# Performance work log

Measured on AMD Instinct MI355X. Metric: run time of the kernel, lower is better.

## Reference

```python
import jax, jax.numpy as jnp
import numpy as np
from jax import lax

DN = ('NHWC', 'HWIO', 'NHWC')
OUTPUT_STRIDE = 2
PEAK_THRESHOLD = 0.2


def setup_inputs() -> dict:
    key = jax.random.key(0)
    k1, k2, k3 = jax.random.split(key, 3)
    crops = jax.random.normal(k1, (128, 192, 192, 1), dtype=jnp.float32)
    # simple confmap backbone: stride-2 conv -> relu -> 3x3 conv to 17 nodes
    W1 = jax.random.normal(k2, (3, 3, 1, 32), dtype=jnp.float32) * 0.1
    b1 = jnp.zeros((32,), dtype=jnp.float32)
    W2 = jax.random.normal(k3, (3, 3, 32, 17), dtype=jnp.float32) * 0.1
    b2 = jnp.zeros((17,), dtype=jnp.float32)
    return {"crops": crops, "W1": W1, "b1": b1, "W2": W2, "b2": b2}


def _confmaps(crops, W1, b1, W2, b2):
    # keras_model forward: (B, 192, 192, 1) -> (B, 96, 96, 17), output_stride = 2
    h = lax.conv_general_dilated(crops, W1, (2, 2), 'SAME', dimension_numbers=DN) + b1
    h = jax.nn.relu(h)
    cms = lax.conv_general_dilated(h, W2, (1, 1), 'SAME', dimension_numbers=DN) + b2
    return cms


def _find_global_peaks_local(cms, threshold):
    # cms: (B, H, W, N) -> peaks (B, N, 2) in (x, y), vals (B, N)
    B, H, W, N = cms.shape
    cm = jnp.transpose(cms, (0, 3, 1, 2)).reshape(B, N, H * W)  # (B, N, HW)
    flat_idx = jnp.argmax(cm, axis=-1)                           # (B, N)
    vals = jnp.take_along_axis(cm, flat_idx[..., None], axis=-1)[..., 0]
    yi = flat_idx // W
    xi = flat_idx % W

    def gather(yy, xx):
        yy = jnp.clip(yy, 0, H - 1)
        xx = jnp.clip(xx, 0, W - 1)
        return jnp.take_along_axis(cm, (yy * W + xx)[..., None], axis=-1)[..., 0]

    # quarter-pixel local gradient offset (refinement='local')
    dx = 0.25 * jnp.sign(gather(yi, xi + 1) - gather(yi, xi - 1))
    dy = 0.25 * jnp.sign(gather(yi + 1, xi) - gather(yi - 1, xi))

    pts = jnp.stack([xi.astype(cm.dtype) + dx, yi.astype(cm.dtype) + dy], axis=-1)
    pts = jnp.where(vals[..., None] >= threshold, pts, jnp.nan)
    return pts, vals


def reference(crops, W1, b1, W2, b2):
    # preprocess: inputs already float grayscale, input_scale=1.0 -> identity
    cms = _confmaps(crops, W1, b1, W2, b2)
    peak_points, peak_vals = _find_global_peaks_local(cms, PEAK_THRESHOLD)
    peak_points = peak_points * OUTPUT_STRIDE  # adjust to input image grid
    # pack (x, y, val) into one array: (B, nodes, 3)
    return jnp.concatenate([peak_points, peak_vals[..., None]], axis=-1)
```

## Files before the change

### kernel.cpp

```cpp
#include <hip/hip_runtime.h>


#define NCH 17
#define C1 32
#define TS2 32
#define HT2 34
#define HS 36
#define IN2 69
#define CG 4
#define NG 8

__device__ __forceinline__ unsigned long long pack_key(float v, unsigned flat) {
    unsigned ub = __float_as_uint(v);
    ub = (ub & 0x80000000u) ? ~ub : (ub | 0x80000000u);
    return ((unsigned long long)ub << 32) | (unsigned)(~flat);
}

__global__ __launch_bounds__(256, 4) void conv_peaks_kernel(
    const float* __restrict__ crops, const float* __restrict__ W1g,
    const float* __restrict__ b1g, const float* __restrict__ W2g,
    const float* __restrict__ b2g, unsigned long long* __restrict__ peaks) {
    __shared__ float s_in[IN2 * IN2];
    __shared__ __align__(16) float s_h[CG * HT2 * HS];

    const int t = threadIdx.x;
    const int b = blockIdx.y;
    const int ty0 = (blockIdx.x / 3) * TS2;
    const int tx0 = (blockIdx.x % 3) * TS2;
    const int iy0 = 2 * ty0 - 2;
    const int ix0 = 2 * tx0 - 2;
    const float* cb = crops + b * 192 * 192;

    for (int p = t; p < IN2 * IN2; p += 256) {
        int r = p / IN2, cc = p - r * IN2;
        int iy = iy0 + r, ix = ix0 + cc;
        float v = 0.f;
        if (iy >= 0 && ix >= 0 && iy < 192 && ix < 192) v = cb[iy * 192 + ix];
        s_in[p] = v;
    }

    const int ly = t >> 3;
    const int lx0 = (t & 7) * 4;
    float acc[NCH][4];
#pragma unroll
    for (int n = 0; n < NCH; ++n)
#pragma unroll
        for (int p = 0; p < 4; ++p) acc[n][p] = 0.f;

#pragma unroll 1
    for (int g = 0; g < NG; ++g) {
        __syncthreads();

        for (int p = t; p < HT2 * HT2; p += 256) {
            int r = p / HT2, cc = p - r * HT2;
            int hy = ty0 - 1 + r, hx = tx0 - 1 + cc;
            bool valid = (hy >= 0) && (hy < 96) && (hx >= 0) && (hx < 96);
            float in9[9];
#pragma unroll
            for (int q = 0; q < 9; ++q)
                in9[q] = s_in[(2 * r + q / 3) * IN2 + (2 * cc + q % 3)];
#pragma unroll
            for (int cl = 0; cl < CG; ++cl) {
                int c = g * CG + cl;
                float a = b1g[c];
#pragma unroll
                for (int q = 0; q < 9; ++q) a = fmaf(in9[q], W1g[q * C1 + c], a);
                a = valid ? fmaxf(a, 0.f) : 0.f;
                s_h[cl * (HT2 * HS) + r * HS + cc] = a;
            }
        }
        __syncthreads();

#pragma unroll 1
        for (int cl = 0; cl < CG; ++cl) {
            float hrow[3][6];
            const float* hp = s_h + cl * (HT2 * HS) + ly * HS + lx0;
#pragma unroll
            for (int r = 0; r < 3; ++r) {
                float4 h4 = *(const float4*)(hp + r * HS);
                float2 h2 = *(const float2*)(hp + r * HS + 4);
                hrow[r][0] = h4.x; hrow[r][1] = h4.y;
                hrow[r][2] = h4.z; hrow[r][3] = h4.w;
                hrow[r][4] = h2.x; hrow[r][5] = h2.y;
            }
            const int c = g * CG + cl;
#pragma unroll
            for (int k = 0; k < 9; ++k) {
                const int ky = k / 3, kx = k - ky * 3;
                const float* wb = W2g + (k * C1 + c) * NCH;
                float w[NCH];
#pragma unroll
                for (int n = 0; n < NCH; ++n) w[n] = wb[n];
#pragma unroll
                for (int n = 0; n < NCH; ++n)
#pragma unroll
                    for (int p = 0; p < 4; ++p)
                        acc[n][p] = fmaf(hrow[ky][kx + p], w[n], acc[n][p]);
            }
        }
    }

    const int yg = ty0 + ly, xg = tx0 + lx0;
    const int lane = t & 63;
#pragma unroll
    for (int n = 0; n < NCH; ++n) {
        float bb = b2g[n];
        unsigned long long pk = pack_key(acc[n][0] + bb, (unsigned)(yg * 96 + xg));
#pragma unroll
        for (int p = 1; p < 4; ++p) {
            unsigned long long o = pack_key(acc[n][p] + bb, (unsigned)(yg * 96 + xg + p));
            if (o > pk) pk = o;
        }
#pragma unroll
        for (int off = 32; off; off >>= 1) {
            unsigned long long o = __shfl_down(pk, off, 64);
            if (o > pk) pk = o;
        }
        if (lane == 0) atomicMax(&peaks[b * NCH + n], pk);
    }
}

__global__ __launch_bounds__(64) void refine_kernel(
    const float* __restrict__ crops, const float* __restrict__ W1g,
    const float* __restrict__ b1g, const float* __restrict__ W2g,
    const unsigned long long* __restrict__ peaks, float* __restrict__ out) {
    const int bn = blockIdx.x;
    const int b = bn / NCH, n = bn % NCH;
    const int lane = threadIdx.x;

    unsigned long long pk = peaks[bn];
    unsigned key = (unsigned)(pk >> 32);
    unsigned fbits = (key & 0x80000000u) ? (key ^ 0x80000000u) : ~key;
    float val = __uint_as_float(fbits);
    int flat = (int)(~(unsigned)(pk & 0xffffffffu));
    int yi = flat / 96, xi = flat - yi * 96;

    const int j = lane >> 4;
    int yy = yi + ((j == 2) ? 1 : 0) - ((j == 3) ? 1 : 0);
    int xx = xi + ((j == 0) ? 1 : 0) - ((j == 1) ? 1 : 0);
    yy = min(max(yy, 0), 95);
    xx = min(max(xx, 0), 95);

    const float* cb = crops + b * 192 * 192;
    float pat[7][7];
#pragma unroll
    for (int r = 0; r < 7; ++r) {
        int iy = 2 * yy - 2 + r;
#pragma unroll
        for (int s = 0; s < 7; ++s) {
            int ix = 2 * xx - 2 + s;
            pat[r][s] = (iy >= 0 && iy < 192 && ix >= 0 && ix < 192)
                            ? cb[iy * 192 + ix] : 0.f;
        }
    }

    float part = 0.f;
#pragma unroll
    for (int ci = 0; ci < 2; ++ci) {
        const int c = (lane & 15) + ci * 16;
        const float bias = b1g[c];
        float w1[9];
#pragma unroll
        for (int q = 0; q < 9; ++q) w1[q] = W1g[q * C1 + c];
#pragma unroll
        for (int dy = 0; dy < 3; ++dy) {
#pragma unroll
            for (int dx = 0; dx < 3; ++dx) {
                int hy = yy - 1 + dy, hx = xx - 1 + dx;
                if (hy >= 0 && hy < 96 && hx >= 0 && hx < 96) {
                    float a = bias;
#pragma unroll
                    for (int qy = 0; qy < 3; ++qy)
#pragma unroll
                        for (int qx = 0; qx < 3; ++qx)
                            a = fmaf(pat[2 * dy + qy][2 * dx + qx],
                                     w1[qy * 3 + qx], a);
                    float hval = fmaxf(a, 0.f);
                    part = fmaf(hval, W2g[((dy * 3 + dx) * C1 + c) * NCH + n], part);
                }
            }
        }
    }
    for (int off = 8; off; off >>= 1) part += __shfl_down(part, off, 16);
    float g0 = __shfl(part, 0, 64);
    float g1 = __shfl(part, 16, 64);
    float g2 = __shfl(part, 32, 64);
    float g3 = __shfl(part, 48, 64);

    if (lane == 0) {
        float d0 = g0 - g1, d1 = g2 - g3;
        float sx = (d0 > 0.f) ? 1.f : ((d0 < 0.f) ? -1.f : 0.f);
        float sy = (d1 > 0.f) ? 1.f : ((d1 < 0.f) ? -1.f : 0.f);
        float px = ((float)xi + 0.25f * sx) * 2.f;
        float py = ((float)yi + 0.25f * sy) * 2.f;
        if (!(val >= 0.2f)) {
            px = __int_as_float(0x7fc00000);
            py = __int_as_float(0x7fc00000);
        }
        out[bn * 3 + 0] = px;
        out[bn * 3 + 1] = py;
        out[bn * 3 + 2] = val;
    }
}

extern "C" void kernel_launch(void* const* d_in, const int* in_sizes, int n_in,
                              void* d_out, int out_size, void* d_ws, size_t ws_size,
                              hipStream_t stream) {
    const float* crops = (const float*)d_in[0];
    const float* W1 = (const float*)d_in[1];
    const float* b1 = (const float*)d_in[2];
    const float* W2 = (const float*)d_in[3];
    const float* b2 = (const float*)d_in[4];
    float* out = (float*)d_out;
    unsigned long long* peaks = (unsigned long long*)d_ws;

    hipMemsetAsync(d_ws, 0, 128 * NCH * sizeof(unsigned long long), stream);

    dim3 gridB(9, 128);
    conv_peaks_kernel<<<gridB, 256, 0, stream>>>(crops, W1, b1, W2, b2, peaks);
    refine_kernel<<<128 * NCH, 64, 0, stream>>>(crops, W1, b1, W2, peaks, out);
}
```

Baseline: 222.3 us.

## Use packed FP32 FMAs and smaller 24x32 tiles for more blocks

Conv2 accumulation now runs on two-wide float vectors (v_pk_fma_f32 on CDNA) over 16 of the 17 output channels, with a scalar FMA for the last one. This targets the FMA issue bottleneck of the second convolution. The tile shrinks to 24x32 with 3 pixels per thread, which raises the grid from 9 to 12 blocks per image to fill more CUs. The trade-off is more halo recompute of conv1 per output pixel and scalar rather than vectorized LDS loads.

```diff
diff --git a/kernel.cpp b/kernel.cpp
--- a/kernel.cpp
+++ b/kernel.cpp
@@ -3,12 +3,17 @@
 
 #define NCH 17
 #define C1 32
-#define TS2 32
-#define HT2 34
-#define HS 36
-#define IN2 69
+#define TW 24
+#define TH 32
+#define HT_W 26
+#define HT_H 34
+#define HSTR 28
+#define IN_W 53
+#define IN_H 69
 #define CG 4
 #define NG 8
+
+typedef float v2f __attribute__((ext_vector_type(2)));
 
 __device__ __forceinline__ unsigned long long pack_key(float v, unsigned flat) {
     unsigned ub = __float_as_uint(v);
@@ -20,19 +25,19 @@
     const float* __restrict__ crops, const float* __restrict__ W1g,
     const float* __restrict__ b1g, const float* __restrict__ W2g,
     const float* __restrict__ b2g, unsigned long long* __restrict__ peaks) {
-    __shared__ float s_in[IN2 * IN2];
-    __shared__ __align__(16) float s_h[CG * HT2 * HS];
+    __shared__ float s_in[IN_H * IN_W];
+    __shared__ __align__(16) float s_h[CG * HT_H * HSTR];
 
     const int t = threadIdx.x;
     const int b = blockIdx.y;
-    const int ty0 = (blockIdx.x / 3) * TS2;
-    const int tx0 = (blockIdx.x % 3) * TS2;
+    const int ty0 = (blockIdx.x >> 2) * TH;
+    const int tx0 = (blockIdx.x & 3) * TW;
     const int iy0 = 2 * ty0 - 2;
     const int ix0 = 2 * tx0 - 2;
     const float* cb = crops + b * 192 * 192;
 
-    for (int p = t; p < IN2 * IN2; p += 256) {
-        int r = p / IN2, cc = p - r * IN2;
+    for (int p = t; p < IN_H * IN_W; p += 256) {
+        int r = p / IN_W, cc = p - r * IN_W;
         int iy = iy0 + r, ix = ix0 + cc;
         float v = 0.f;
         if (iy >= 0 && ix >= 0 && iy < 192 && ix < 192) v = cb[iy * 192 + ix];
@@ -40,25 +45,28 @@
     }
 
     const int ly = t >> 3;
-    const int lx0 = (t & 7) * 4;
-    float acc[NCH][4];
-#pragma unroll
-    for (int n = 0; n < NCH; ++n)
-#pragma unroll
-        for (int p = 0; p < 4; ++p) acc[n][p] = 0.f;
+    const int lx0 = (t & 7) * 3;
+    v2f acc2[8][3];
+    float acc1[3];
+#pragma unroll
+    for (int m = 0; m < 8; ++m)
+#pragma unroll
+        for (int p = 0; p < 3; ++p) acc2[m][p] = (v2f)(0.f);
+#pragma unroll
+    for (int p = 0; p < 3; ++p) acc1[p] = 0.f;
 
 #pragma unroll 1
     for (int g = 0; g < NG; ++g) {
         __syncthreads();
 
-        for (int p = t; p < HT2 * HT2; p += 256) {
-            int r = p / HT2, cc = p - r * HT2;
+        for (int p = t; p < HT_H * HT_W; p += 256) {
+            int r = p / HT_W, cc = p - r * HT_W;
             int hy = ty0 - 1 + r, hx = tx0 - 1 + cc;
             bool valid = (hy >= 0) && (hy < 96) && (hx >= 0) && (hx < 96);
             float in9[9];
 #pragma unroll
             for (int q = 0; q < 9; ++q)
-                in9[q] = s_in[(2 * r + q / 3) * IN2 + (2 * cc + q % 3)];
+                in9[q] = s_in[(2 * r + q / 3) * IN_W + (2 * cc + q % 3)];
 #pragma unroll
             for (int cl = 0; cl < CG; ++cl) {
                 int c = g * CG + cl;
@@ -66,23 +74,19 @@
 #pragma unroll
                 for (int q = 0; q < 9; ++q) a = fmaf(in9[q], W1g[q * C1 + c], a);
                 a = valid ? fmaxf(a, 0.f) : 0.f;
-                s_h[cl * (HT2 * HS) + r * HS + cc] = a;
+                s_h[cl * (HT_H * HSTR) + r * HSTR + cc] = a;
             }
         }
         __syncthreads();
 
 #pragma unroll 1
         for (int cl = 0; cl < CG; ++cl) {
-            float hrow[3][6];
-            const float* hp = s_h + cl * (HT2 * HS) + ly * HS + lx0;
-#pragma unroll
-            for (int r = 0; r < 3; ++r) {
-                float4 h4 = *(const float4*)(hp + r * HS);
-                float2 h2 = *(const float2*)(hp + r * HS + 4);
-                hrow[r][0] = h4.x; hrow[r][1] = h4.y;
-                hrow[r][2] = h4.z; hrow[r][3] = h4.w;
-                hrow[r][4] = h2.x; hrow[r][5] = h2.y;
-            }
+            float hrow[3][5];
+            const float* hp = s_h + cl * (HT_H * HSTR) + ly * HSTR + lx0;
+#pragma unroll
+            for (int r = 0; r < 3; ++r)
+#pragma unroll
+                for (int j = 0; j < 5; ++j) hrow[r][j] = hp[r * HSTR + j];
             const int c = g * CG + cl;
 #pragma unroll
             for (int k = 0; k < 9; ++k) {
@@ -91,11 +95,18 @@
                 float w[NCH];
 #pragma unroll
                 for (int n = 0; n < NCH; ++n) w[n] = wb[n];
-#pragma unroll
-                for (int n = 0; n < NCH; ++n)
-#pragma unroll
-                    for (int p = 0; p < 4; ++p)
-                        acc[n][p] = fmaf(hrow[ky][kx + p], w[n], acc[n][p]);
+                v2f wp[8];
+#pragma unroll
+                for (int m = 0; m < 8; ++m) wp[m] = (v2f){w[2 * m], w[2 * m + 1]};
+#pragma unroll
+                for (int p = 0; p < 3; ++p) {
+                    const float h = hrow[ky][kx + p];
+                    const v2f hh = {h, h};
+#pragma unroll
+                    for (int m = 0; m < 8; ++m)
+                        acc2[m][p] = __builtin_elementwise_fma(hh, wp[m], acc2[m][p]);
+                    acc1[p] = fmaf(h, w[16], acc1[p]);
+                }
             }
         }
     }
@@ -104,11 +115,15 @@
     const int lane = t & 63;
 #pragma unroll
     for (int n = 0; n < NCH; ++n) {
-        float bb = b2g[n];
-        unsigned long long pk = pack_key(acc[n][0] + bb, (unsigned)(yg * 96 + xg));
-#pragma unroll
-        for (int p = 1; p < 4; ++p) {
-            unsigned long long o = pack_key(acc[n][p] + bb, (unsigned)(yg * 96 + xg + p));
+        const float bb = b2g[n];
+        float v_[3];
+#pragma unroll
+        for (int p = 0; p < 3; ++p)
+            v_[p] = ((n < 16) ? acc2[n >> 1][p][n & 1] : acc1[p]) + bb;
+        unsigned long long pk = pack_key(v_[0], (unsigned)(yg * 96 + xg));
+#pragma unroll
+        for (int p = 1; p < 3; ++p) {
+            unsigned long long o = pack_key(v_[p], (unsigned)(yg * 96 + xg + p));
             if (o > pk) pk = o;
         }
 #pragma unroll
@@ -216,7 +231,7 @@
 
     hipMemsetAsync(d_ws, 0, 128 * NCH * sizeof(unsigned long long), stream);
 
-    dim3 gridB(9, 128);
+    dim3 gridB(12, 128);
     conv_peaks_kernel<<<gridB, 256, 0, stream>>>(crops, W1, b1, W2, b2, peaks);
     refine_kernel<<<128 * NCH, 64, 0, stream>>>(crops, W1, b1, W2, peaks, out);
 }
```

After: 207.7 us. -6.6%, faster.
